# Optimization experiments

Measured on AMD Instinct MI355X. Metric: run time of the kernel, lower is better.

Reference implementation:

```python
import jax, jax.numpy as jnp
import numpy as np

N_NODES = 20000
N_EDGES = 160000
D = 1000          # out_channels of GatedGraphConv / Linear in-dim
NUM_LAYERS = 3


def setup_inputs() -> dict:
    key = jax.random.key(0)
    ks = jax.random.split(key, 10)
    x = jax.random.normal(ks[0], (N_NODES, D), dtype=jnp.float32)
    edge_index = jax.random.randint(ks[1], (2, N_EDGES), 0, N_NODES, dtype=jnp.int32)
    edge_weight = jax.random.uniform(ks[2], (N_EDGES,), dtype=jnp.float32)
    s = 1.0 / np.sqrt(D)
    weight = jax.random.uniform(ks[3], (NUM_LAYERS, D, D), minval=-s, maxval=s, dtype=jnp.float32)
    w_ih = jax.random.uniform(ks[4], (3 * D, D), minval=-s, maxval=s, dtype=jnp.float32)
    w_hh = jax.random.uniform(ks[5], (3 * D, D), minval=-s, maxval=s, dtype=jnp.float32)
    b_ih = jax.random.uniform(ks[6], (3 * D,), minval=-s, maxval=s, dtype=jnp.float32)
    b_hh = jax.random.uniform(ks[7], (3 * D,), minval=-s, maxval=s, dtype=jnp.float32)
    fc_w = jax.random.uniform(ks[8], (1, D), minval=-s, maxval=s, dtype=jnp.float32)
    fc_b = jax.random.uniform(ks[9], (1,), minval=-s, maxval=s, dtype=jnp.float32)
    return {
        "x": x, "edge_index": edge_index, "edge_weight": edge_weight,
        "weight": weight, "w_ih": w_ih, "w_hh": w_hh, "b_ih": b_ih, "b_hh": b_hh,
        "fc_w": fc_w, "fc_b": fc_b, "prob": 0,
    }


def _gru_cell(m, h, w_ih, w_hh, b_ih, b_hh):
    # torch.nn.GRUCell: gate order r, z, n
    gi = m @ w_ih.T + b_ih   # [N, 3D]
    gh = h @ w_hh.T + b_hh   # [N, 3D]
    i_r, i_z, i_n = jnp.split(gi, 3, axis=-1)
    h_r, h_z, h_n = jnp.split(gh, 3, axis=-1)
    r = jax.nn.sigmoid(i_r + h_r)
    z = jax.nn.sigmoid(i_z + h_z)
    n = jnp.tanh(i_n + r * h_n)
    return (1.0 - z) * n + z * h


def reference(x, edge_index, edge_weight, weight, w_ih, w_hh, b_ih, b_hh, fc_w, fc_b, prob):
    src = edge_index[0]
    dst = edge_index[1]
    h = x
    for layer in range(NUM_LAYERS):
        m = h @ weight[layer]                                  # [N, D]
        msg = m[src] * edge_weight[:, None]                    # [E, D]
        agg = jax.ops.segment_sum(msg, dst, num_segments=N_NODES)  # scatter-add
        h = _gru_cell(agg, h, w_ih, w_hh, b_ih, b_hh)
    h = jax.nn.relu(h)
    # F.dropout with p=prob=0 is identity (scale 1/(1-0)=1)
    return h @ fc_w.T + fc_b                                   # [N, 1]
```

## Files before the change

### kernel.cpp

```cpp
#include <hip/hip_runtime.h>

typedef unsigned short u16;
typedef unsigned int u32;
typedef __attribute__((ext_vector_type(8))) short bf16x8;
typedef __attribute__((ext_vector_type(4))) float f32x4;

#define N_NODES 20000
#define N_EDGES 160000
#define DDIM    1000
#define KP      1024
#define SP      41200000
#define WCAT_L  6291456

__device__ __forceinline__ float b2f(u16 u) {
    union { u32 i; float f; } v; v.i = ((u32)u) << 16; return v.f;
}
__device__ __forceinline__ u16 f2b(float f) {
    union { float f; u32 i; } v; v.f = f;
    u32 r = v.i + 0x7FFFu + ((v.i >> 16) & 1u);
    return (u16)(r >> 16);
}
__device__ __forceinline__ u32 pack2(float a, float b) {
    return (u32)f2b(a) | ((u32)f2b(b) << 16);
}
__device__ __forceinline__ f32x4 mfma16(bf16x8 a, bf16x8 b, f32x4 c) {
    return __builtin_amdgcn_mfma_f32_16x16x32_bf16(a, b, c, 0, 0, 0);
}
__device__ __forceinline__ float fexp_(float x) {
    return __builtin_amdgcn_exp2f(x * 1.4426950408889634f);
}
__device__ __forceinline__ float fsigmoid_(float x) {
    return __builtin_amdgcn_rcpf(1.0f + fexp_(-x));
}
__device__ __forceinline__ float ftanh_(float x) {
    float ax = fabsf(x);
    float e = fexp_(-2.0f * ax);
    float t = (1.0f - e) * __builtin_amdgcn_rcpf(1.0f + e);
    return x >= 0.0f ? t : -t;
}

__device__ __forceinline__ void gl2lds16(const u16* g, u16* l) {
    __builtin_amdgcn_global_load_lds(
        (const __attribute__((address_space(1))) u32*)g,
        (__attribute__((address_space(3))) u32*)l, 16, 0, 0);
}

__global__ __launch_bounds__(256) void cvt_rows(const float* __restrict__ in,
                                                u16* __restrict__ out) {
    int r = blockIdx.x, c = threadIdx.x * 4;
    u32 o[2] = {0, 0};
    if (c < DDIM) {
        float4 v = *(const float4*)(in + (size_t)r * DDIM + c);
        o[0] = pack2(v.x, v.y); o[1] = pack2(v.z, v.w);
    }
    *(uint2*)(out + (size_t)r * KP + c) = *(const uint2*)o;
}

__global__ __launch_bounds__(256) void cvt_weights(const float* __restrict__ wih,
                                                   const float* __restrict__ W,
                                                   const float* __restrict__ whh,
                                                   u16* __restrict__ wihb,
                                                   u16* __restrict__ Wb3,
                                                   u16* __restrict__ wcat) {
    int b = blockIdx.x, c = threadIdx.x * 4;
    const float* src;
    u16* dst;
    if (b < 3000) {
        src = wih + (size_t)b * DDIM;
        dst = wihb + (size_t)b * KP;
    } else if (b < 6000) {
        int r = b - 3000;
        int l = r / 1000, row = r - l * 1000;
        src = W + (size_t)r * DDIM;
        dst = Wb3 + (size_t)l * 1048576 + (size_t)row * KP;
    } else {
        int r = b - 6000;
        int l = r / 3000, gr = r - l * 3000;
        int g = gr / 1000, n2 = gr - g * 1000;
        src = whh + (size_t)gr * DDIM;
        dst = wcat + (size_t)l * WCAT_L + ((size_t)g * 1024 + n2) * 2048 + 1024;
    }
    u32 o[2] = {0, 0};
    if (c < DDIM) {
        float4 v = *(const float4*)(src + c);
        o[0] = pack2(v.x, v.y); o[1] = pack2(v.z, v.w);
    }
    *(uint2*)(dst + c) = *(const uint2*)o;
}

__global__ __launch_bounds__(256) void count_edges(const int* __restrict__ ei,
                                                   int* __restrict__ cnt) {
    int e = blockIdx.x * 256 + threadIdx.x;
    if (e < N_EDGES) atomicAdd(&cnt[ei[N_EDGES + e]], 1);
}

__global__ __launch_bounds__(1024) void scan_offsets(const int* __restrict__ cnt,
                                                     int* __restrict__ ofs) {
    __shared__ int s[1024];
    const int CH = 20;
    int t = threadIdx.x;
    int base = t * CH;
    int loc[CH];
    int sum = 0;
    for (int j = 0; j < CH; j++) {
        int i = base + j;
        loc[j] = sum;
        sum += (i < N_NODES) ? cnt[i] : 0;
    }
    s[t] = sum;
    __syncthreads();
    for (int d = 1; d < 1024; d <<= 1) {
        int v = (t >= d) ? s[t - d] : 0;
        __syncthreads();
        s[t] += v;
        __syncthreads();
    }
    int excl = s[t] - sum;
    for (int j = 0; j < CH; j++) {
        int i = base + j;
        if (i < N_NODES) ofs[i] = excl + loc[j];
    }
    if (t == 0) ofs[N_NODES] = N_EDGES;
}

__global__ __launch_bounds__(256) void fill_buckets(const int* __restrict__ ei,
                                                    const int* __restrict__ ofs,
                                                    int* __restrict__ cur,
                                                    int* __restrict__ bkt) {
    int e = blockIdx.x * 256 + threadIdx.x;
    if (e >= N_EDGES) return;
    int d = ei[N_EDGES + e];
    int pos = atomicAdd(&cur[d], 1);
    bkt[ofs[d] + pos] = e;
}

__global__ __launch_bounds__(256) void node_agg(const int* __restrict__ ei,
                                                const float* __restrict__ ew,
                                                const int* __restrict__ ofs,
                                                const int* __restrict__ bkt,
                                                const u16* __restrict__ hsrc,
                                                u16* __restrict__ agg) {
    __shared__ int   s_src[2][32];
    __shared__ float s_w[2][32];
    __shared__ int   s_it[2];
    int tid = threadIdx.x;
    int half = tid >> 7, t = tid & 127;
    int node = blockIdx.x * 2 + half;
    int beg = ofs[node], end = ofs[node + 1];
    if (t == 0) s_it[half] = (end - beg + 31) >> 5;
    __syncthreads();
    int iters = max(s_it[0], s_it[1]);
    float acc[8] = {};
    for (int it = 0; it < iters; it++) {
        int cb = beg + it * 32;
        int n = min(32, end - cb);
        if (t < n) {
            int e = bkt[cb + t];
            s_src[half][t] = ei[e];
            s_w[half][t]   = ew[e];
        }
        __syncthreads();
        if (t < 125) {
            for (int j = 0; j < n; j++) {
                int src = s_src[half][j];
                float w = s_w[half][j];
                uint4 v = *(const uint4*)(hsrc + (size_t)src * KP + t * 8);
                const u16* p = (const u16*)&v;
#pragma unroll
                for (int k = 0; k < 8; k++) acc[k] += b2f(p[k]) * w;
            }
        }
        __syncthreads();
    }
    if (t < 125) {
        u32 o[4] = {pack2(acc[0], acc[1]), pack2(acc[2], acc[3]),
                    pack2(acc[4], acc[5]), pack2(acc[6], acc[7])};
        *(uint4*)(agg + (size_t)node * KP + t * 8) = *(const uint4*)o;
    } else if (t < 128) {
        uint4 z = {0, 0, 0, 0};
        *(uint4*)(agg + (size_t)node * KP + 1000 + (t - 125) * 8) = z;
    }
}

__global__ __launch_bounds__(256) void gemm_wc(const u16* __restrict__ A,
                                               const u16* __restrict__ Bt3,
                                               u16* __restrict__ wcat) {
    __shared__ u16 S[16384];
    int tid = threadIdx.x;
    int lane = tid & 63, wave = tid >> 6;
    int wr = wave >> 1, wc = wave & 1;
    int bid = blockIdx.x;
    int l = blockIdx.y;
    int m0 = (bid >> 3) * 128, n0 = (bid & 7) * 128;
    const u16* Bt = Bt3 + (size_t)l * 1048576;

    int aoff[4], boff[4];
#pragma unroll
    for (int i = 0; i < 4; i++) {
        int c = tid + 256 * i;
        int row = c >> 3, sl = c & 7;
        int kc = sl ^ (row & 7);
        aoff[i] = (m0 + row) * KP + kc * 8;
        boff[i] = (n0 + row) * KP + kc * 8;
    }
    f32x4 acc[4][4] = {};
    int fr = lane & 15, q = lane >> 4, sw = fr & 7;

    for (int k0 = 0; k0 < KP; k0 += 64) {
#pragma unroll
        for (int i = 0; i < 4; i++) {
            gl2lds16(A + aoff[i] + k0, &S[tid * 8 + 2048 * i]);
            gl2lds16(Bt + boff[i] + k0, &S[8192 + tid * 8 + 2048 * i]);
        }
        __syncthreads();
#pragma unroll
        for (int ks = 0; ks < 2; ks++) {
            int kx = ((ks * 4 + q) ^ sw) * 8;
            bf16x8 af[4], bf[4];
#pragma unroll
            for (int i = 0; i < 4; i++)
                af[i] = *(const bf16x8*)&S[(wr * 64 + i * 16 + fr) * 64 + kx];
#pragma unroll
            for (int j = 0; j < 4; j++)
                bf[j] = *(const bf16x8*)&S[8192 + (wc * 64 + j * 16 + fr) * 64 + kx];
#pragma unroll
            for (int i = 0; i < 4; i++)
#pragma unroll
                for (int j = 0; j < 4; j++)
                    acc[i][j] = mfma16(af[i], bf[j], acc[i][j]);
        }
        __syncthreads();
    }

    u16* wl = wcat + (size_t)l * WCAT_L;
    int cc = lane & 15, r4 = q * 4;
#pragma unroll
    for (int i = 0; i < 4; i++)
#pragma unroll
        for (int j = 0; j < 4; j++) {
            int gn = n0 + wc * 64 + j * 16 + cc;
            if (gn >= DDIM) continue;
#pragma unroll
            for (int r = 0; r < 4; r++) {
                int gm = m0 + wr * 64 + i * 16 + r4 + r;
                if (gm >= 3000) continue;
                int slab = (gm >= 2000) ? 2 : (gm >= 1000 ? 1 : 0);
                int row = gm - slab * 1000;
                wl[(size_t)slab * 2097152 + (size_t)row * 2048 + gn] =
                    f2b(acc[i][j][r]);
            }
        }
}

__global__ __launch_bounds__(256) void gru_fused(const u16* __restrict__ agg,
                                                 const u16* __restrict__ h,
                                                 const u16* __restrict__ wcat,
                                                 const float* __restrict__ bih,
                                                 const float* __restrict__ bhh,
                                                 u16* __restrict__ hout) {
    __shared__ u16 S[20480];
    int tid = threadIdx.x;
    int lane = tid & 63, wave = tid >> 6;
    int wr = wave >> 1, wc = wave & 1;

    int bid = blockIdx.x;
    int xcd = bid & 7;
    int s = bid >> 3;
    int hi = (s >= 157) ? 1 : 0;
    int m0 = (s - hi * 157) * 128;
    int n0 = (xcd * 2 + hi) * 64;

    int aoff[4], woff[2];
#pragma unroll
    for (int i = 0; i < 4; i++) {
        int c = tid + 256 * i;
        int row = c >> 3, sl = c & 7;
        int kc = sl ^ (row & 7);
        aoff[i] = (m0 + row) * KP + kc * 8;
    }
#pragma unroll
    for (int i = 0; i < 2; i++) {
        int c = tid + 256 * i;
        int row = (c >> 3) & 63, sl = c & 7;
        int kc = sl ^ (row & 7);
        woff[i] = (n0 + row) * 2048 + kc * 8;
    }
    f32x4 aR[4][2] = {}, aZ[4][2] = {}, aN[4][2] = {}, aH[4][2] = {};
    int fr = lane & 15, q = lane >> 4, sw = fr & 7;

#define GRU_PHASE(APTR, K0W, AN)                                              \
    for (int kk = 0; kk < 16; kk++) {                                         \
        int ka = kk * 64, kw = K0W + kk * 64;                                 \
        _Pragma("unroll")                                                     \
        for (int i = 0; i < 4; i++)                                           \
            gl2lds16(APTR + aoff[i] + ka, &S[tid * 8 + 2048 * i]);            \
        _Pragma("unroll")                                                     \
        for (int i = 0; i < 2; i++) {                                         \
            gl2lds16(wcat + woff[i] + kw, &S[8192 + tid * 8 + 2048 * i]);     \
            gl2lds16(wcat + 2097152 + woff[i] + kw,                           \
                     &S[12288 + tid * 8 + 2048 * i]);                         \
            gl2lds16(wcat + 4194304 + woff[i] + kw,                           \
                     &S[16384 + tid * 8 + 2048 * i]);                         \
        }                                                                     \
        __syncthreads();                                                      \
        _Pragma("unroll")                                                     \
        for (int ks = 0; ks < 2; ks++) {                                      \
            int kx = ((ks * 4 + q) ^ sw) * 8;                                 \
            bf16x8 aa[4], w0[2], w1[2], w2[2];                                \
            _Pragma("unroll")                                                 \
            for (int i = 0; i < 4; i++)                                       \
                aa[i] = *(const bf16x8*)&S[(wr * 64 + i * 16 + fr) * 64 + kx];\
            _Pragma("unroll")                                                 \
            for (int j = 0; j < 2; j++) {                                     \
                int rb = (wc * 32 + j * 16 + fr) * 64 + kx;                   \
                w0[j] = *(const bf16x8*)&S[8192 + rb];                        \
                w1[j] = *(const bf16x8*)&S[12288 + rb];                       \
                w2[j] = *(const bf16x8*)&S[16384 + rb];                       \
            }                                                                 \
            _Pragma("unroll")                                                 \
            for (int i = 0; i < 4; i++)                                       \
                _Pragma("unroll")                                             \
                for (int j = 0; j < 2; j++) {                                 \
                    aR[i][j] = mfma16(aa[i], w0[j], aR[i][j]);                \
                    aZ[i][j] = mfma16(aa[i], w1[j], aZ[i][j]);                \
                    AN[i][j] = mfma16(aa[i], w2[j], AN[i][j]);                \
                }                                                             \
        }                                                                     \
        __syncthreads();                                                      \
    }

    GRU_PHASE(agg, 0, aN)
    GRU_PHASE(h, 1024, aH)
#undef GRU_PHASE

    int cc = lane & 15, r4 = q * 4;
#pragma unroll
    for (int j = 0; j < 2; j++) {
        int gn = n0 + wc * 32 + j * 16 + cc;
        if (gn >= DDIM) continue;
        float br  = bih[gn] + bhh[gn];
        float bz  = bih[1000 + gn] + bhh[1000 + gn];
        float bni = bih[2000 + gn];
        float bnh = bhh[2000 + gn];
#pragma unroll
        for (int i = 0; i < 4; i++)
#pragma unroll
            for (int r = 0; r < 4; r++) {
                int gm = m0 + wr * 64 + i * 16 + r4 + r;
                if (gm >= N_NODES) continue;
                float rg = fsigmoid_(aR[i][j][r] + br);
                float zg = fsigmoid_(aZ[i][j][r] + bz);
                float ng = ftanh_(aN[i][j][r] + bni + rg * (aH[i][j][r] + bnh));
                size_t idx = (size_t)gm * KP + gn;
                float hp = b2f(h[idx]);
                hout[idx] = f2b((1.0f - zg) * ng + zg * hp);
            }
    }
}

__global__ __launch_bounds__(256) void fc_out(const u16* __restrict__ h,
                                              const float* __restrict__ fw,
                                              const float* __restrict__ fb,
                                              float* __restrict__ out) {
    int row = blockIdx.x * 4 + (threadIdx.x >> 6);
    int lane = threadIdx.x & 63;
    if (row >= N_NODES) return;
    float s = 0.0f;
#pragma unroll
    for (int i = 0; i < 2; i++) {
        int c = lane + 64 * i;
        if (c < 125) {
            uint4 v = *(const uint4*)(h + (size_t)row * KP + c * 8);
            const u16* pv = (const u16*)&v;
            float4 w0 = *(const float4*)(fw + c * 8);
            float4 w1 = *(const float4*)(fw + c * 8 + 4);
            const float* wp = (const float*)&w0;
            float hv;
#pragma unroll
            for (int k = 0; k < 4; k++) {
                hv = b2f(pv[k]);
                s += (hv > 0.0f ? hv : 0.0f) * wp[k];
            }
            wp = (const float*)&w1;
#pragma unroll
            for (int k = 0; k < 4; k++) {
                hv = b2f(pv[4 + k]);
                s += (hv > 0.0f ? hv : 0.0f) * wp[k];
            }
        }
    }
    for (int off = 32; off > 0; off >>= 1) s += __shfl_down(s, off, 64);
    if (lane == 0) out[row] = s + fb[0];
}

extern "C" void kernel_launch(void* const* d_in, const int* in_sizes, int n_in,
                              void* d_out, int out_size, void* d_ws, size_t ws_size,
                              hipStream_t stream) {
    const float* x   = (const float*)d_in[0];
    const int*   ei  = (const int*)d_in[1];
    const float* ew  = (const float*)d_in[2];
    const float* W   = (const float*)d_in[3];
    const float* wih = (const float*)d_in[4];
    const float* whh = (const float*)d_in[5];
    const float* bih = (const float*)d_in[6];
    const float* bhh = (const float*)d_in[7];
    const float* fw  = (const float*)d_in[8];
    const float* fb  = (const float*)d_in[9];
    float* out = (float*)d_out;

    char* ws = (char*)d_ws;
    u16* xb   = (u16*)(ws);
    u16* bufA = (u16*)(ws + (size_t)SP);
    u16* bufB = (u16*)(ws + (size_t)2 * SP);
    u16* wcat = (u16*)(ws + 123600000);
    int* cnt  = (int*)(ws + 161400000);
    int* cur  = (int*)(ws + 161480000);
    int* ofs  = (int*)(ws + 161560000);
    int* bkt  = (int*)(ws + 161640192);

    u16* wihb = bufA;
    u16* Wb3  = bufA + 3145728;

    cvt_rows<<<N_NODES, 256, 0, stream>>>(x, xb);
    cvt_weights<<<15000, 256, 0, stream>>>(wih, W, whh, wihb, Wb3, wcat);
    gemm_wc<<<dim3(192, 3), 256, 0, stream>>>(wihb, Wb3, wcat);
    hipMemsetAsync(cnt, 0, 160000, stream);
    count_edges<<<625, 256, 0, stream>>>(ei, cnt);
    scan_offsets<<<1, 1024, 0, stream>>>(cnt, ofs);
    fill_buckets<<<625, 256, 0, stream>>>(ei, ofs, cur, bkt);

    node_agg<<<10000, 256, 0, stream>>>(ei, ew, ofs, bkt, xb, bufB);
    gru_fused<<<2512, 256, 0, stream>>>(bufB, xb, wcat, bih, bhh, bufA);

    node_agg<<<10000, 256, 0, stream>>>(ei, ew, ofs, bkt, bufA, bufB);
    gru_fused<<<2512, 256, 0, stream>>>(bufB, bufA, wcat + WCAT_L, bih, bhh, xb);

    node_agg<<<10000, 256, 0, stream>>>(ei, ew, ofs, bkt, xb, bufB);
    gru_fused<<<2512, 256, 0, stream>>>(bufB, xb, wcat + 2 * WCAT_L, bih, bhh, bufA);

    fc_out<<<5000, 256, 0, stream>>>(bufA, fw, fb, out);
}
```

Baseline: 1.276 ms.

## Restructure GRU GEMM into 512-thread 256-row tiles with triple-buffered LDS pipeline

```diff
diff --git a/kernel.cpp b/kernel.cpp
--- a/kernel.cpp
+++ b/kernel.cpp
@@ -252,101 +252,133 @@
         }
 }
 
-__global__ __launch_bounds__(256) void gru_fused(const u16* __restrict__ agg,
-                                                 const u16* __restrict__ h,
-                                                 const u16* __restrict__ wcat,
-                                                 const float* __restrict__ bih,
-                                                 const float* __restrict__ bhh,
-                                                 u16* __restrict__ hout) {
-    __shared__ u16 S[20480];
+__global__ __launch_bounds__(512, 2) void gru_fused(const u16* __restrict__ agg,
+                                                    const u16* __restrict__ h,
+                                                    const u16* __restrict__ wcat,
+                                                    const float* __restrict__ bih,
+                                                    const float* __restrict__ bhh,
+                                                    u16* __restrict__ hout) {
+    extern __shared__ u16 S[];
     int tid = threadIdx.x;
     int lane = tid & 63, wave = tid >> 6;
-    int wr = wave >> 1, wc = wave & 1;
 
     int bid = blockIdx.x;
     int xcd = bid & 7;
     int s = bid >> 3;
-    int hi = (s >= 157) ? 1 : 0;
-    int m0 = (s - hi * 157) * 128;
+    int panel = s >> 1, hi = s & 1;
+    int m0 = panel * 256;
     int n0 = (xcd * 2 + hi) * 64;
 
-    int aoff[4], woff[2];
+    int aoff[4];
 #pragma unroll
     for (int i = 0; i < 4; i++) {
-        int c = tid + 256 * i;
+        int c = tid + 512 * i;
         int row = c >> 3, sl = c & 7;
         int kc = sl ^ (row & 7);
         aoff[i] = (m0 + row) * KP + kc * 8;
     }
-#pragma unroll
-    for (int i = 0; i < 2; i++) {
-        int c = tid + 256 * i;
-        int row = (c >> 3) & 63, sl = c & 7;
-        int kc = sl ^ (row & 7);
-        woff[i] = (n0 + row) * 2048 + kc * 8;
-    }
-    f32x4 aR[4][2] = {}, aZ[4][2] = {}, aN[4][2] = {}, aH[4][2] = {};
+    int wrow = tid >> 3;
+    int woff = (n0 + wrow) * 2048 + ((tid & 7) ^ (wrow & 7)) * 8;
+
+    f32x4 aR[2][4] = {}, aZ[2][4] = {}, aN[2][4] = {}, aH[2][4] = {};
     int fr = lane & 15, q = lane >> 4, sw = fr & 7;
-
-#define GRU_PHASE(APTR, K0W, AN)                                              \
-    for (int kk = 0; kk < 16; kk++) {                                         \
-        int ka = kk * 64, kw = K0W + kk * 64;                                 \
+    int arow = (wave * 32 + fr) * 64;
+    int wfr = fr * 64;
+    int kx0 = (q ^ sw) * 8, kx1 = ((4 + q) ^ sw) * 8;
+
+#define STAGE_W(ts, wb) do {                                                  \
+        int kw_ = (ts) * 64;                                                  \
         _Pragma("unroll")                                                     \
-        for (int i = 0; i < 4; i++)                                           \
-            gl2lds16(APTR + aoff[i] + ka, &S[tid * 8 + 2048 * i]);            \
+        for (int g_ = 0; g_ < 3; g_++)                                        \
+            gl2lds16(wcat + (size_t)g_ * 2097152 + woff + kw_,                \
+                     &S[49152 + (wb) * 12288 + g_ * 4096 + tid * 8]);         \
+    } while (0)
+
+#define STAGE_A2(ts, ab, r0) do {                                             \
+        const u16* ap_ = ((ts) < 16) ? agg : h;                               \
+        int kb_ = ((ts) < 16) ? (ts) * 64 : (ts) * 64 - 1024;                 \
         _Pragma("unroll")                                                     \
-        for (int i = 0; i < 2; i++) {                                         \
-            gl2lds16(wcat + woff[i] + kw, &S[8192 + tid * 8 + 2048 * i]);     \
-            gl2lds16(wcat + 2097152 + woff[i] + kw,                           \
-                     &S[12288 + tid * 8 + 2048 * i]);                         \
-            gl2lds16(wcat + 4194304 + woff[i] + kw,                           \
-                     &S[16384 + tid * 8 + 2048 * i]);                         \
+        for (int i_ = (r0); i_ < (r0) + 2; i_++)                              \
+            gl2lds16(ap_ + aoff[i_] + kb_,                                    \
+                     &S[(ab) * 16384 + tid * 8 + 4096 * i_]);                 \
+    } while (0)
+
+#define READ_WF(g_) do {                                                      \
+        _Pragma("unroll")                                                     \
+        for (int j_ = 0; j_ < 4; j_++) {                                      \
+            wf[j_][0] = *(const bf16x8*)&S[Wb + (g_) * 4096 + wfr + j_ * 1024 + kx0]; \
+            wf[j_][1] = *(const bf16x8*)&S[Wb + (g_) * 4096 + wfr + j_ * 1024 + kx1]; \
         }                                                                     \
-        __syncthreads();                                                      \
+    } while (0)
+
+#define MFMA_PH(ACC) do {                                                     \
+        __builtin_amdgcn_s_setprio(1);                                        \
         _Pragma("unroll")                                                     \
-        for (int ks = 0; ks < 2; ks++) {                                      \
-            int kx = ((ks * 4 + q) ^ sw) * 8;                                 \
-            bf16x8 aa[4], w0[2], w1[2], w2[2];                                \
+        for (int i_ = 0; i_ < 2; i_++)                                        \
             _Pragma("unroll")                                                 \
-            for (int i = 0; i < 4; i++)                                       \
-                aa[i] = *(const bf16x8*)&S[(wr * 64 + i * 16 + fr) * 64 + kx];\
-            _Pragma("unroll")                                                 \
-            for (int j = 0; j < 2; j++) {                                     \
-                int rb = (wc * 32 + j * 16 + fr) * 64 + kx;                   \
-                w0[j] = *(const bf16x8*)&S[8192 + rb];                        \
-                w1[j] = *(const bf16x8*)&S[12288 + rb];                       \
-                w2[j] = *(const bf16x8*)&S[16384 + rb];                       \
+            for (int j_ = 0; j_ < 4; j_++) {                                  \
+                ACC[i_][j_] = mfma16(af[i_][0], wf[j_][0], ACC[i_][j_]);      \
+                ACC[i_][j_] = mfma16(af[i_][1], wf[j_][1], ACC[i_][j_]);      \
             }                                                                 \
-            _Pragma("unroll")                                                 \
-            for (int i = 0; i < 4; i++)                                       \
-                _Pragma("unroll")                                             \
-                for (int j = 0; j < 2; j++) {                                 \
-                    aR[i][j] = mfma16(aa[i], w0[j], aR[i][j]);                \
-                    aZ[i][j] = mfma16(aa[i], w1[j], aZ[i][j]);                \
-                    AN[i][j] = mfma16(aa[i], w2[j], AN[i][j]);                \
-                }                                                             \
-        }                                                                     \
-        __syncthreads();                                                      \
-    }
-
-    GRU_PHASE(agg, 0, aN)
-    GRU_PHASE(h, 1024, aH)
-#undef GRU_PHASE
+        __builtin_amdgcn_s_setprio(0);                                        \
+    } while (0)
+
+    STAGE_A2(0, 0, 0); STAGE_A2(0, 0, 2);
+    STAGE_W(0, 0);
+    STAGE_A2(1, 1, 0); STAGE_A2(1, 1, 2);
+    asm volatile("s_waitcnt vmcnt(4)" ::: "memory");
+    __builtin_amdgcn_s_barrier();
+
+    int abuf = 0;
+#pragma unroll 1
+    for (int t = 0; t < 32; t++) {
+        int Ab = abuf * 16384;
+        int Wb = 49152 + (t & 1) * 12288;
+        bf16x8 af[2][2], wf[4][2];
+#pragma unroll
+        for (int i_ = 0; i_ < 2; i_++) {
+            af[i_][0] = *(const bf16x8*)&S[Ab + arow + i_ * 1024 + kx0];
+            af[i_][1] = *(const bf16x8*)&S[Ab + arow + i_ * 1024 + kx1];
+        }
+        READ_WF(0);
+        if (t <= 30) STAGE_W(t + 1, (t + 1) & 1);
+        __builtin_amdgcn_s_barrier();
+        MFMA_PH(aR);
+        __builtin_amdgcn_s_barrier();
+        READ_WF(1);
+        int anext = abuf + 2; if (anext >= 3) anext -= 3;
+        if (t <= 29) STAGE_A2(t + 2, anext, 0);
+        __builtin_amdgcn_s_barrier();
+        MFMA_PH(aZ);
+        __builtin_amdgcn_s_barrier();
+        READ_WF(2);
+        if (t <= 29) STAGE_A2(t + 2, anext, 2);
+        __builtin_amdgcn_s_barrier();
+        if (t < 16) MFMA_PH(aN); else MFMA_PH(aH);
+        if (t <= 29)      asm volatile("s_waitcnt vmcnt(4)" ::: "memory");
+        else if (t == 30) asm volatile("s_waitcnt vmcnt(0)" ::: "memory");
+        __builtin_amdgcn_s_barrier();
+        abuf++; if (abuf == 3) abuf = 0;
+    }
+#undef STAGE_W
+#undef STAGE_A2
+#undef READ_WF
+#undef MFMA_PH
 
     int cc = lane & 15, r4 = q * 4;
 #pragma unroll
-    for (int j = 0; j < 2; j++) {
-        int gn = n0 + wc * 32 + j * 16 + cc;
+    for (int j = 0; j < 4; j++) {
+        int gn = n0 + j * 16 + cc;
         if (gn >= DDIM) continue;
         float br  = bih[gn] + bhh[gn];
         float bz  = bih[1000 + gn] + bhh[1000 + gn];
         float bni = bih[2000 + gn];
         float bnh = bhh[2000 + gn];
 #pragma unroll
-        for (int i = 0; i < 4; i++)
+        for (int i = 0; i < 2; i++)
 #pragma unroll
             for (int r = 0; r < 4; r++) {
-                int gm = m0 + wr * 64 + i * 16 + r4 + r;
+                int gm = m0 + wave * 32 + i * 16 + r4 + r;
                 if (gm >= N_NODES) continue;
                 float rg = fsigmoid_(aR[i][j][r] + br);
                 float zg = fsigmoid_(aZ[i][j][r] + bz);
@@ -408,6 +440,9 @@
     const float* fb  = (const float*)d_in[9];
     float* out = (float*)d_out;
 
+    hipFuncSetAttribute((const void*)gru_fused,
+                        hipFuncAttributeMaxDynamicSharedMemorySize, 147456);
+
     char* ws = (char*)d_ws;
     u16* xb   = (u16*)(ws);
     u16* bufA = (u16*)(ws + (size_t)SP);
@@ -430,13 +465,13 @@
     fill_buckets<<<625, 256, 0, stream>>>(ei, ofs, cur, bkt);
 
     node_agg<<<10000, 256, 0, stream>>>(ei, ew, ofs, bkt, xb, bufB);
-    gru_fused<<<2512, 256, 0, stream>>>(bufB, xb, wcat, bih, bhh, bufA);
+    gru_fused<<<1264, 512, 147456, stream>>>(bufB, xb, wcat, bih, bhh, bufA);
 
     node_agg<<<10000, 256, 0, stream>>>(ei, ew, ofs, bkt, bufA, bufB);
-    gru_fused<<<2512, 256, 0, stream>>>(bufB, bufA, wcat + WCAT_L, bih, bhh, xb);
+    gru_fused<<<1264, 512, 147456, stream>>>(bufB, bufA, wcat + WCAT_L, bih, bhh, xb);
 
     node_agg<<<10000, 256, 0, stream>>>(ei, ew, ofs, bkt, xb, bufB);
-    gru_fused<<<2512, 256, 0, stream>>>(bufB, xb, wcat + 2 * WCAT_L, bih, bhh, bufA);
+    gru_fused<<<1264, 512, 147456, stream>>>(bufB, xb, wcat + 2 * WCAT_L, bih, bhh, bufA);
 
     fc_out<<<5000, 256, 0, stream>>>(bufA, fw, fb, out);
 }
```

Measured after the change: 1.219 ms. -4.4%, faster.
